# Kernel tuning notes

Hardware: AMD Instinct MI355X
Metric: run time of the kernel (lower is better)

Reference implementation:

```python
import jax, jax.numpy as jnp
import numpy as np

N_NODES = 100000
N_EDGES = 3200000
D_IN = 256
D_OUT = 256


def setup_inputs() -> dict:
    key = jax.random.key(0)
    k1, k2, k3, k4, k5 = jax.random.split(key, 5)
    x = jax.random.normal(k1, (N_NODES, D_IN), dtype=jnp.float32)
    W = jax.random.normal(k2, (D_OUT, D_IN), dtype=jnp.float32) * (1.0 / np.sqrt(D_IN))
    edge_val = jax.random.uniform(k3, (N_EDGES,), dtype=jnp.float32)
    edge_row = jax.random.randint(k4, (N_EDGES,), 0, N_NODES, dtype=jnp.int32)
    edge_col = jax.random.randint(k5, (N_EDGES,), 0, N_NODES, dtype=jnp.int32)
    return {"x": x, "W": W, "edge_val": edge_val, "edge_row": edge_row, "edge_col": edge_col}


def reference(x, W, edge_val, edge_row, edge_col):
    # Linear (no bias): [N, D_in] @ [D_in, D_out] -> [N, D_out]
    h = x @ W.T
    # SpMM: out[r] = sum_e val[e] * h[col[e]] for edges with row[e] == r
    msgs = h[edge_col] * edge_val[:, None]          # [E, D_out] gather + scale
    out = jax.ops.segment_sum(msgs, edge_row, num_segments=N_NODES)  # scatter-add
    return out
```

## Files before the change

### kernel.cpp

```cpp
#include <hip/hip_runtime.h>
#include <hip/hip_bf16.h>

typedef float  f32x4 __attribute__((ext_vector_type(4)));
typedef short  s16x8 __attribute__((ext_vector_type(8)));
typedef unsigned short u16x8 __attribute__((ext_vector_type(8)));

#define N_NODES 100000
#define N_EDGES 3200000
#define DD 256

#define ROWS_PER_BKT 128
#define NBKT 782
#define BKT_CAP 4608
#define ACHUNK 3072
#define NABLK 1042
#define EDGES_PER_THREAD 12

#define BM 64
#define BN 256
#define BK 64
#define LDA 72
#define GEMM_BLOCKS 1563

#define K1_LDS (4*NBKT*4 + 256*4 + ACHUNK*8 + ACHUNK*4)
#define QBLOCKS 1024

__device__ __forceinline__ ushort f2bf(float f) {
    union { __hip_bfloat16 b; ushort u; } cv;
    cv.b = __float2bfloat16(f);
    return cv.u;
}
__device__ __forceinline__ float bf2f(ushort u) {
    return __uint_as_float(((unsigned)u) << 16);
}

__global__ __launch_bounds__(256) void wconv_kernel(const float* __restrict__ w, ushort* __restrict__ wb)
{
    int gid = blockIdx.x * 256 + threadIdx.x;
    float4 a = ((const float4*)w)[gid * 2];
    float4 b = ((const float4*)w)[gid * 2 + 1];
    u16x8 o = { f2bf(a.x), f2bf(a.y), f2bf(a.z), f2bf(a.w),
                f2bf(b.x), f2bf(b.y), f2bf(b.z), f2bf(b.w) };
    ((u16x8*)wb)[gid] = o;
}

__global__ __launch_bounds__(256) void k1_kernel(
    const float* __restrict__ x, const ushort* __restrict__ wb, ushort* __restrict__ h,
    const int* __restrict__ erow, const int* __restrict__ ecol,
    const float* __restrict__ eval, int* __restrict__ gcur,
    int2* __restrict__ pairsA)
{
    extern __shared__ char smem[];
    const int tid = threadIdx.x;

    if (blockIdx.x < GEMM_BLOCKS) {
        ushort (*xs)[LDA]  = (ushort(*)[LDA])smem;
        ushort (*wsx)[LDA] = (ushort(*)[LDA])(smem + BM * LDA * 2);
        const int lane = tid & 63;
        const int wq   = tid >> 6;
        const int bm   = blockIdx.x * BM;
        const int l15 = lane & 15;
        const int lhi = lane >> 4;
        f32x4 acc[4][4] = {};

        for (int k0 = 0; k0 < DD; k0 += BK) {
            #pragma unroll
            for (int it = 0; it < 4; ++it) {
                int f = (it * 256 + tid) * 4;
                int r = f >> 6, c = f & 63;
                float4 v = make_float4(0.f, 0.f, 0.f, 0.f);
                if (bm + r < N_NODES) v = *(const float4*)(x + (size_t)(bm + r) * DD + k0 + c);
                *(ushort4*)&xs[r][c] = make_ushort4(f2bf(v.x), f2bf(v.y), f2bf(v.z), f2bf(v.w));
            }
            #pragma unroll
            for (int it = 0; it < 8; ++it) {
                int f = (it * 256 + tid) * 8;
                int r = f >> 6, c = f & 63;
                *(uint4*)&wsx[r][c] = *(const uint4*)(wb + (size_t)r * DD + k0 + c);
            }
            __syncthreads();
            #pragma unroll
            for (int kk = 0; kk < 2; ++kk) {
                const int koff = kk * 32 + lhi * 8;
                s16x8 a[4], b[4];
                #pragma unroll
                for (int m = 0; m < 4; ++m)
                    a[m] = *(const s16x8*)&xs[m * 16 + l15][koff];
                #pragma unroll
                for (int n = 0; n < 4; ++n)
                    b[n] = *(const s16x8*)&wsx[wq * 64 + n * 16 + l15][koff];
                #pragma unroll
                for (int m = 0; m < 4; ++m)
                    #pragma unroll
                    for (int n = 0; n < 4; ++n)
                        acc[m][n] = __builtin_amdgcn_mfma_f32_16x16x32_bf16(a[m], b[n], acc[m][n], 0, 0, 0);
            }
            __syncthreads();
        }
        #pragma unroll
        for (int m = 0; m < 4; ++m)
            #pragma unroll
            for (int n = 0; n < 4; ++n)
                #pragma unroll
                for (int r = 0; r < 4; ++r) {
                    int row = bm + m * 16 + lhi * 4 + r;
                    int col = wq * 64 + n * 16 + l15;
                    if (row < N_NODES) h[(size_t)row * DD + col] = f2bf(acc[m][n][r]);
                }
        return;
    }

    int*  hist   = (int*)smem;
    int*  sbase  = hist  + NBKT;
    int*  scur   = sbase + NBKT;
    int*  rbase  = scur  + NBKT;
    int*  gsum   = rbase + NBKT;
    int2* staged = (int2*)(gsum + 256);
    int*  gdst   = (int*)(staged + ACHUNK);

    for (int i = tid; i < NBKT; i += 256) hist[i] = 0;
    __syncthreads();
    const int base = (blockIdx.x - GEMM_BLOCKS) * ACHUNK;
    int pk[EDGES_PER_THREAD]; float vv[EDGES_PER_THREAD]; int bk[EDGES_PER_THREAD];
    #pragma unroll
    for (int k = 0; k < EDGES_PER_THREAD; ++k) {
        int i = base + k * 256 + tid;
        bk[k] = -1;
        if (i < N_EDGES) {
            int r = erow[i];
            bk[k] = r >> 7;
            pk[k] = ecol[i] | ((r & 127) << 17);
            vv[k] = eval[i];
            atomicAdd(&hist[bk[k]], 1);
        }
    }
    __syncthreads();
    int gs = 0, lv[4];
    #pragma unroll
    for (int j = 0; j < 4; ++j) {
        int b = tid * 4 + j;
        lv[j] = (b < NBKT) ? hist[b] : 0;
        gs += lv[j];
    }
    gsum[tid] = gs;
    __syncthreads();
    for (int s = 1; s < 256; s <<= 1) {
        int t = (tid >= s) ? gsum[tid - s] : 0;
        __syncthreads();
        gsum[tid] += t;
        __syncthreads();
    }
    int run = gsum[tid] - gs;
    #pragma unroll
    for (int j = 0; j < 4; ++j) {
        int b = tid * 4 + j;
        if (b < NBKT) { sbase[b] = run; scur[b] = run; }
        run += lv[j];
    }
    __syncthreads();
    for (int b = tid; b < NBKT; b += 256) {
        int c = hist[b];
        if (c) rbase[b] = atomicAdd(&gcur[b], c);
    }
    __syncthreads();
    #pragma unroll
    for (int k = 0; k < EDGES_PER_THREAD; ++k) {
        if (bk[k] >= 0) {
            int lo = atomicAdd(&scur[bk[k]], 1);
            staged[lo] = make_int2(pk[k], __float_as_int(vv[k]));
            gdst[lo] = bk[k] * BKT_CAP + rbase[bk[k]] + (lo - sbase[bk[k]]);
        }
    }
    __syncthreads();
    const int cnt = min(ACHUNK, N_EDGES - base);
    for (int t = tid; t < cnt; t += 256)
        pairsA[gdst[t]] = staged[t];
}

__global__ __launch_bounds__(256) void quant_kernel(
    const ushort* __restrict__ h, unsigned char* __restrict__ h8,
    float* __restrict__ hscale)
{
    const int w    = blockIdx.x * 4 + (threadIdx.x >> 6);
    const int lane = threadIdx.x & 63;
    for (int row = w; row < N_NODES; row += QBLOCKS * 4) {
        ushort4 hv = *(const ushort4*)(h + (size_t)row * DD + lane * 4);
        float f0 = bf2f(hv.x), f1 = bf2f(hv.y), f2 = bf2f(hv.z), f3 = bf2f(hv.w);
        float m = fmaxf(fmaxf(fabsf(f0), fabsf(f1)), fmaxf(fabsf(f2), fabsf(f3)));
        #pragma unroll
        for (int s = 1; s < 64; s <<= 1)
            m = fmaxf(m, __shfl_xor(m, s));
        m = fmaxf(m, 1e-30f);
        const float sc = 127.0f * __builtin_amdgcn_rcpf(m);
        int q0 = (int)rintf(f0 * sc), q1 = (int)rintf(f1 * sc);
        int q2 = (int)rintf(f2 * sc), q3 = (int)rintf(f3 * sc);
        unsigned pack = (q0 & 255) | ((q1 & 255) << 8) | ((q2 & 255) << 16) | ((unsigned)(q3 & 255) << 24);
        *(unsigned*)(h8 + (size_t)row * DD + lane * 4) = pack;
        if (lane == 0) hscale[row] = m * (1.0f / 127.0f);
    }
}

__global__ __launch_bounds__(256) void passB_kernel(
    const int2* __restrict__ pairsA, const int* __restrict__ gcur,
    int2* __restrict__ pairsB, int2* __restrict__ row_se)
{
    __shared__ int hist[ROWS_PER_BKT];
    __shared__ int lds[ROWS_PER_BKT];
    __shared__ int cur[ROWS_PER_BKT];
    const int tid = threadIdx.x;
    const int b = blockIdx.x;
    const int cnt = gcur[b];
    const int base = b * BKT_CAP;
    if (tid < ROWS_PER_BKT) hist[tid] = 0;
    __syncthreads();
    for (int i = tid; i < cnt; i += 256)
        atomicAdd(&hist[(pairsA[base + i].x >> 17) & 127], 1);
    __syncthreads();
    int v = (tid < ROWS_PER_BKT) ? hist[tid] : 0;
    if (tid < ROWS_PER_BKT) lds[tid] = v;
    __syncthreads();
    for (int st = 1; st < ROWS_PER_BKT; st <<= 1) {
        int t = (tid >= st && tid < ROWS_PER_BKT) ? lds[tid - st] : 0;
        __syncthreads();
        if (tid < ROWS_PER_BKT) lds[tid] += t;
        __syncthreads();
    }
    if (tid < ROWS_PER_BKT) {
        int excl = lds[tid] - v;
        int r = b * ROWS_PER_BKT + tid;
        if (r < N_NODES) row_se[r] = make_int2(base + excl, base + excl + v);
        cur[tid] = base + excl;
    }
    __syncthreads();
    for (int i = tid; i < cnt; i += 256) {
        int2 p = pairsA[base + i];
        int rl = (p.x >> 17) & 127;
        int d = atomicAdd(&cur[rl], 1);
        pairsB[d] = make_int2(p.x & 0x1FFFF, p.y);
    }
}

__global__ __launch_bounds__(256) void spmm_kernel(
    const unsigned char* __restrict__ h8, const float* __restrict__ hscale,
    const int2* __restrict__ pairs, const int2* __restrict__ row_se,
    float* __restrict__ out)
{
    const int wid  = blockIdx.x * 4 + (threadIdx.x >> 6);
    const int lane = threadIdx.x & 63;
    if (wid >= N_NODES) return;
    const int2 se = row_se[wid];
    const int s = __builtin_amdgcn_readfirstlane(se.x);
    const int e = __builtin_amdgcn_readfirstlane(se.y);
    const int loff = lane * 4;
    float ax = 0.f, ay = 0.f, az = 0.f, aw = 0.f;

    int j = s;
    for (; j + 8 <= e; j += 8) {
        const int4* p4 = (const int4*)(pairs + j);
        int4 q0 = p4[0], q1 = p4[1], q2 = p4[2], q3 = p4[3];
        int   c[8] = { q0.x, q0.z, q1.x, q1.z, q2.x, q2.z, q3.x, q3.z };
        float v[8] = { __int_as_float(q0.y), __int_as_float(q0.w),
                       __int_as_float(q1.y), __int_as_float(q1.w),
                       __int_as_float(q2.y), __int_as_float(q2.w),
                       __int_as_float(q3.y), __int_as_float(q3.w) };
        float vs[8];
        #pragma unroll
        for (int t = 0; t < 8; ++t) vs[t] = v[t] * hscale[c[t]];
        unsigned hv[8];
        #pragma unroll
        for (int t = 0; t < 8; ++t)
            hv[t] = *(const unsigned*)(h8 + (size_t)c[t] * DD + loff);
        #pragma unroll
        for (int t = 0; t < 8; ++t) {
            ax += vs[t] * (float)((int)(hv[t] << 24) >> 24);
            ay += vs[t] * (float)((int)(hv[t] << 16) >> 24);
            az += vs[t] * (float)((int)(hv[t] <<  8) >> 24);
            aw += vs[t] * (float)((int)hv[t] >> 24);
        }
    }
    for (; j < e; ++j) {
        int2 p = pairs[j];
        const float vs = __int_as_float(p.y) * hscale[p.x];
        const unsigned hv = *(const unsigned*)(h8 + (size_t)p.x * DD + loff);
        ax += vs * (float)((int)(hv << 24) >> 24);
        ay += vs * (float)((int)(hv << 16) >> 24);
        az += vs * (float)((int)(hv <<  8) >> 24);
        aw += vs * (float)((int)hv >> 24);
    }
    f32x4 o = { ax, ay, az, aw };
    __builtin_nontemporal_store(o, (f32x4*)(out + (size_t)wid * DD + loff));
}

extern "C" void kernel_launch(void* const* d_in, const int* in_sizes, int n_in,
                              void* d_out, int out_size, void* d_ws, size_t ws_size,
                              hipStream_t stream)
{
    const float* x        = (const float*)d_in[0];
    const float* W        = (const float*)d_in[1];
    const float* edge_val = (const float*)d_in[2];
    const int*   edge_row = (const int*)d_in[3];
    const int*   edge_col = (const int*)d_in[4];
    float* out = (float*)d_out;

    char* ws = (char*)d_ws;
    size_t off = 0;
    auto alloc = [&](size_t bytes) {
        void* p = ws + off;
        off = (off + bytes + 255) & ~(size_t)255;
        return p;
    };
    unsigned char* h8     = (unsigned char*)alloc((size_t)N_NODES * DD);
    float*         hscale = (float*)alloc((size_t)N_NODES * sizeof(float));
    int2*          pairsA = (int2*)alloc((size_t)NBKT * BKT_CAP * sizeof(int2));
    int2*          pairsB = (int2*)alloc((size_t)NBKT * BKT_CAP * sizeof(int2));
    ushort*        wb     = (ushort*)alloc((size_t)DD * DD * sizeof(ushort));
    int*           gcur   = (int*)alloc((size_t)NBKT * sizeof(int));
    int2*          row_se = (int2*)alloc((size_t)N_NODES * sizeof(int2));
    (void)ws_size;

    ushort* h = (ushort*)d_out;

    (void)hipMemsetAsync(gcur, 0, (size_t)NBKT * sizeof(int), stream);

    wconv_kernel<<<DD * DD / 8 / 256, 256, 0, stream>>>(W, wb);

    k1_kernel<<<GEMM_BLOCKS + NABLK, 256, K1_LDS, stream>>>(
        x, wb, h, edge_row, edge_col, edge_val, gcur, pairsA);

    quant_kernel<<<QBLOCKS, 256, 0, stream>>>(h, h8, hscale);

    passB_kernel<<<NBKT, 256, 0, stream>>>(pairsA, gcur, pairsB, row_se);

    int spmm_blocks = (N_NODES + 3) / 4;
    spmm_kernel<<<spmm_blocks, 256, 0, stream>>>(h8, hscale, pairsB, row_se, out);
}
```

Before: 253.8 us.

## Split GEMM from edge binning, fuse quantization with pass B

The GEMM no longer shares a launch with the edge-binning pass A. Each now runs as its own kernel with static LDS sizing, so the GEMM blocks stop reserving pass A's large LDS footprint. The GEMM tile shrinks to 64x128 and uses twice as many blocks, each wave computing a 32x64 sub-tile. Quantization and pass B merge into one heterogeneous launch so the two independent phases overlap. The trade-off is that GEMM and pass A now run serially instead of concurrently, and the smaller tile reloads each x tile twice.

```diff
diff --git a/kernel.cpp b/kernel.cpp
--- a/kernel.cpp
+++ b/kernel.cpp
@@ -16,14 +16,13 @@
 #define NABLK 1042
 #define EDGES_PER_THREAD 12
 
-#define BM 64
-#define BN 256
-#define BK 64
-#define LDA 72
-#define GEMM_BLOCKS 1563
-
-#define K1_LDS (4*NBKT*4 + 256*4 + ACHUNK*8 + ACHUNK*4)
-#define QBLOCKS 1024
+#define GBM 64
+#define GBN 128
+#define GBK 64
+#define GLDA 72
+#define GEMM_BLOCKS 3126
+
+#define QB_BLOCKS 1024
 
 __device__ __forceinline__ ushort f2bf(float f) {
     union { __hip_bfloat16 b; ushort u; } cv;
@@ -44,83 +43,83 @@
     ((u16x8*)wb)[gid] = o;
 }
 
-__global__ __launch_bounds__(256) void k1_kernel(
-    const float* __restrict__ x, const ushort* __restrict__ wb, ushort* __restrict__ h,
+__global__ __launch_bounds__(256) void gemm_kernel(
+    const float* __restrict__ x, const ushort* __restrict__ wb, ushort* __restrict__ h)
+{
+    __shared__ ushort xs[GBM][GLDA];
+    __shared__ ushort wsx[GBN][GLDA];
+    const int tid  = threadIdx.x;
+    const int lane = tid & 63;
+    const int wave = tid >> 6;
+    const int wr = wave >> 1, wc = wave & 1;
+    const int bm = (blockIdx.x >> 1) * GBM;
+    const int bn = (blockIdx.x & 1) * GBN;
+    const int l15 = lane & 15;
+    const int lhi = lane >> 4;
+    f32x4 acc[2][4] = {};
+
+    for (int k0 = 0; k0 < DD; k0 += GBK) {
+        #pragma unroll
+        for (int it = 0; it < 4; ++it) {
+            int f = (it * 256 + tid) * 4;
+            int r = f >> 6, c = f & 63;
+            float4 v = make_float4(0.f, 0.f, 0.f, 0.f);
+            if (bm + r < N_NODES) v = *(const float4*)(x + (size_t)(bm + r) * DD + k0 + c);
+            *(ushort4*)&xs[r][c] = make_ushort4(f2bf(v.x), f2bf(v.y), f2bf(v.z), f2bf(v.w));
+        }
+        #pragma unroll
+        for (int it = 0; it < 4; ++it) {
+            int f = (it * 256 + tid) * 8;
+            int r = f >> 6, c = f & 63;
+            *(uint4*)&wsx[r][c] = *(const uint4*)(wb + (size_t)(bn + r) * DD + k0 + c);
+        }
+        __syncthreads();
+        #pragma unroll
+        for (int kk = 0; kk < 2; ++kk) {
+            const int koff = kk * 32 + lhi * 8;
+            s16x8 a[2], b[4];
+            #pragma unroll
+            for (int m = 0; m < 2; ++m)
+                a[m] = *(const s16x8*)&xs[wr * 32 + m * 16 + l15][koff];
+            #pragma unroll
+            for (int n = 0; n < 4; ++n)
+                b[n] = *(const s16x8*)&wsx[wc * 64 + n * 16 + l15][koff];
+            #pragma unroll
+            for (int m = 0; m < 2; ++m)
+                #pragma unroll
+                for (int n = 0; n < 4; ++n)
+                    acc[m][n] = __builtin_amdgcn_mfma_f32_16x16x32_bf16(a[m], b[n], acc[m][n], 0, 0, 0);
+        }
+        __syncthreads();
+    }
+    #pragma unroll
+    for (int m = 0; m < 2; ++m)
+        #pragma unroll
+        for (int n = 0; n < 4; ++n)
+            #pragma unroll
+            for (int r = 0; r < 4; ++r) {
+                int row = bm + wr * 32 + m * 16 + lhi * 4 + r;
+                int col = bn + wc * 64 + n * 16 + l15;
+                if (row < N_NODES) h[(size_t)row * DD + col] = f2bf(acc[m][n][r]);
+            }
+}
+
+__global__ __launch_bounds__(256) void passA_kernel(
     const int* __restrict__ erow, const int* __restrict__ ecol,
     const float* __restrict__ eval, int* __restrict__ gcur,
     int2* __restrict__ pairsA)
 {
-    extern __shared__ char smem[];
+    __shared__ int hist[NBKT];
+    __shared__ int sbase[NBKT];
+    __shared__ int scur[NBKT];
+    __shared__ int rbase[NBKT];
+    __shared__ int gsum[256];
+    __shared__ int2 staged[ACHUNK];
+    __shared__ int gdst[ACHUNK];
     const int tid = threadIdx.x;
-
-    if (blockIdx.x < GEMM_BLOCKS) {
-        ushort (*xs)[LDA]  = (ushort(*)[LDA])smem;
-        ushort (*wsx)[LDA] = (ushort(*)[LDA])(smem + BM * LDA * 2);
-        const int lane = tid & 63;
-        const int wq   = tid >> 6;
-        const int bm   = blockIdx.x * BM;
-        const int l15 = lane & 15;
-        const int lhi = lane >> 4;
-        f32x4 acc[4][4] = {};
-
-        for (int k0 = 0; k0 < DD; k0 += BK) {
-            #pragma unroll
-            for (int it = 0; it < 4; ++it) {
-                int f = (it * 256 + tid) * 4;
-                int r = f >> 6, c = f & 63;
-                float4 v = make_float4(0.f, 0.f, 0.f, 0.f);
-                if (bm + r < N_NODES) v = *(const float4*)(x + (size_t)(bm + r) * DD + k0 + c);
-                *(ushort4*)&xs[r][c] = make_ushort4(f2bf(v.x), f2bf(v.y), f2bf(v.z), f2bf(v.w));
-            }
-            #pragma unroll
-            for (int it = 0; it < 8; ++it) {
-                int f = (it * 256 + tid) * 8;
-                int r = f >> 6, c = f & 63;
-                *(uint4*)&wsx[r][c] = *(const uint4*)(wb + (size_t)r * DD + k0 + c);
-            }
-            __syncthreads();
-            #pragma unroll
-            for (int kk = 0; kk < 2; ++kk) {
-                const int koff = kk * 32 + lhi * 8;
-                s16x8 a[4], b[4];
-                #pragma unroll
-                for (int m = 0; m < 4; ++m)
-                    a[m] = *(const s16x8*)&xs[m * 16 + l15][koff];
-                #pragma unroll
-                for (int n = 0; n < 4; ++n)
-                    b[n] = *(const s16x8*)&wsx[wq * 64 + n * 16 + l15][koff];
-                #pragma unroll
-                for (int m = 0; m < 4; ++m)
-                    #pragma unroll
-                    for (int n = 0; n < 4; ++n)
-                        acc[m][n] = __builtin_amdgcn_mfma_f32_16x16x32_bf16(a[m], b[n], acc[m][n], 0, 0, 0);
-            }
-            __syncthreads();
-        }
-        #pragma unroll
-        for (int m = 0; m < 4; ++m)
-            #pragma unroll
-            for (int n = 0; n < 4; ++n)
-                #pragma unroll
-                for (int r = 0; r < 4; ++r) {
-                    int row = bm + m * 16 + lhi * 4 + r;
-                    int col = wq * 64 + n * 16 + l15;
-                    if (row < N_NODES) h[(size_t)row * DD + col] = f2bf(acc[m][n][r]);
-                }
-        return;
-    }
-
-    int*  hist   = (int*)smem;
-    int*  sbase  = hist  + NBKT;
-    int*  scur   = sbase + NBKT;
-    int*  rbase  = scur  + NBKT;
-    int*  gsum   = rbase + NBKT;
-    int2* staged = (int2*)(gsum + 256);
-    int*  gdst   = (int*)(staged + ACHUNK);
-
     for (int i = tid; i < NBKT; i += 256) hist[i] = 0;
     __syncthreads();
-    const int base = (blockIdx.x - GEMM_BLOCKS) * ACHUNK;
+    const int base = blockIdx.x * ACHUNK;
     int pk[EDGES_PER_THREAD]; float vv[EDGES_PER_THREAD]; int bk[EDGES_PER_THREAD];
     #pragma unroll
     for (int k = 0; k < EDGES_PER_THREAD; ++k) {
@@ -177,13 +176,54 @@
         pairsA[gdst[t]] = staged[t];
 }
 
-__global__ __launch_bounds__(256) void quant_kernel(
+__global__ __launch_bounds__(256) void qb_kernel(
+    const int2* __restrict__ pairsA, const int* __restrict__ gcur,
+    int2* __restrict__ pairsB, int2* __restrict__ row_se,
     const ushort* __restrict__ h, unsigned char* __restrict__ h8,
     float* __restrict__ hscale)
 {
-    const int w    = blockIdx.x * 4 + (threadIdx.x >> 6);
-    const int lane = threadIdx.x & 63;
-    for (int row = w; row < N_NODES; row += QBLOCKS * 4) {
+    __shared__ int hist[ROWS_PER_BKT];
+    __shared__ int lds[ROWS_PER_BKT];
+    __shared__ int cur[ROWS_PER_BKT];
+    const int tid = threadIdx.x;
+
+    if (blockIdx.x < NBKT) {
+        const int b = blockIdx.x;
+        const int cnt = gcur[b];
+        const int base = b * BKT_CAP;
+        if (tid < ROWS_PER_BKT) hist[tid] = 0;
+        __syncthreads();
+        for (int i = tid; i < cnt; i += 256)
+            atomicAdd(&hist[(pairsA[base + i].x >> 17) & 127], 1);
+        __syncthreads();
+        int v = (tid < ROWS_PER_BKT) ? hist[tid] : 0;
+        if (tid < ROWS_PER_BKT) lds[tid] = v;
+        __syncthreads();
+        for (int st = 1; st < ROWS_PER_BKT; st <<= 1) {
+            int t = (tid >= st && tid < ROWS_PER_BKT) ? lds[tid - st] : 0;
+            __syncthreads();
+            if (tid < ROWS_PER_BKT) lds[tid] += t;
+            __syncthreads();
+        }
+        if (tid < ROWS_PER_BKT) {
+            int excl = lds[tid] - v;
+            int r = b * ROWS_PER_BKT + tid;
+            if (r < N_NODES) row_se[r] = make_int2(base + excl, base + excl + v);
+            cur[tid] = base + excl;
+        }
+        __syncthreads();
+        for (int i = tid; i < cnt; i += 256) {
+            int2 p = pairsA[base + i];
+            int rl = (p.x >> 17) & 127;
+            int d = atomicAdd(&cur[rl], 1);
+            pairsB[d] = make_int2(p.x & 0x1FFFF, p.y);
+        }
+        return;
+    }
+
+    const int w    = (blockIdx.x - NBKT) * 4 + (tid >> 6);
+    const int lane = tid & 63;
+    for (int row = w; row < N_NODES; row += QB_BLOCKS * 4) {
         ushort4 hv = *(const ushort4*)(h + (size_t)row * DD + lane * 4);
         float f0 = bf2f(hv.x), f1 = bf2f(hv.y), f2 = bf2f(hv.z), f3 = bf2f(hv.w);
         float m = fmaxf(fmaxf(fabsf(f0), fabsf(f1)), fmaxf(fabsf(f2), fabsf(f3)));
@@ -197,46 +237,6 @@
         unsigned pack = (q0 & 255) | ((q1 & 255) << 8) | ((q2 & 255) << 16) | ((unsigned)(q3 & 255) << 24);
         *(unsigned*)(h8 + (size_t)row * DD + lane * 4) = pack;
         if (lane == 0) hscale[row] = m * (1.0f / 127.0f);
-    }
-}
-
-__global__ __launch_bounds__(256) void passB_kernel(
-    const int2* __restrict__ pairsA, const int* __restrict__ gcur,
-    int2* __restrict__ pairsB, int2* __restrict__ row_se)
-{
-    __shared__ int hist[ROWS_PER_BKT];
-    __shared__ int lds[ROWS_PER_BKT];
-    __shared__ int cur[ROWS_PER_BKT];
-    const int tid = threadIdx.x;
-    const int b = blockIdx.x;
-    const int cnt = gcur[b];
-    const int base = b * BKT_CAP;
-    if (tid < ROWS_PER_BKT) hist[tid] = 0;
-    __syncthreads();
-    for (int i = tid; i < cnt; i += 256)
-        atomicAdd(&hist[(pairsA[base + i].x >> 17) & 127], 1);
-    __syncthreads();
-    int v = (tid < ROWS_PER_BKT) ? hist[tid] : 0;
-    if (tid < ROWS_PER_BKT) lds[tid] = v;
-    __syncthreads();
-    for (int st = 1; st < ROWS_PER_BKT; st <<= 1) {
-        int t = (tid >= st && tid < ROWS_PER_BKT) ? lds[tid - st] : 0;
-        __syncthreads();
-        if (tid < ROWS_PER_BKT) lds[tid] += t;
-        __syncthreads();
-    }
-    if (tid < ROWS_PER_BKT) {
-        int excl = lds[tid] - v;
-        int r = b * ROWS_PER_BKT + tid;
-        if (r < N_NODES) row_se[r] = make_int2(base + excl, base + excl + v);
-        cur[tid] = base + excl;
-    }
-    __syncthreads();
-    for (int i = tid; i < cnt; i += 256) {
-        int2 p = pairsA[base + i];
-        int rl = (p.x >> 17) & 127;
-        int d = atomicAdd(&cur[rl], 1);
-        pairsB[d] = make_int2(p.x & 0x1FFFF, p.y);
     }
 }
 
@@ -324,12 +324,11 @@
 
     wconv_kernel<<<DD * DD / 8 / 256, 256, 0, stream>>>(W, wb);
 
-    k1_kernel<<<GEMM_BLOCKS + NABLK, 256, K1_LDS, stream>>>(
-        x, wb, h, edge_row, edge_col, edge_val, gcur, pairsA);
-
-    quant_kernel<<<QBLOCKS, 256, 0, stream>>>(h, h8, hscale);
-
-    passB_kernel<<<NBKT, 256, 0, stream>>>(pairsA, gcur, pairsB, row_se);
+    gemm_kernel<<<GEMM_BLOCKS, 256, 0, stream>>>(x, wb, h);
+
+    passA_kernel<<<NABLK, 256, 0, stream>>>(edge_row, edge_col, edge_val, gcur, pairsA);
+
+    qb_kernel<<<NBKT + QB_BLOCKS, 256, 0, stream>>>(pairsA, gcur, pairsB, row_se, h, h8, hscale);
 
     int spmm_blocks = (N_NODES + 3) / 4;
     spmm_kernel<<<spmm_blocks, 256, 0, stream>>>(h8, hscale, pairsB, row_se, out);
```

Measured after the change: 288.0 us. +13.4%, slower.
